# Kernel tuning notes

Measured on AMD Instinct MI355X. Metric: run time of the kernel, lower is better.

The kernel has to match this reference:

```python
import jax, jax.numpy as jnp
import numpy as np

H = 1024   # hiddenDim
L = 3      # numLayers


def _cell(x, h, c, Wih, Whh, bih, bhh):
    """One LSTM cell step, PyTorch gate order (i, f, g, o)."""
    gates = x @ Wih.T + bih + h @ Whh.T + bhh
    i, f, g, o = jnp.split(gates, 4, axis=-1)
    c = jax.nn.sigmoid(f) * c + jax.nn.sigmoid(i) * jnp.tanh(g)
    h = jax.nn.sigmoid(o) * jnp.tanh(c)
    return h, c


def _layer(xs, Wih, Whh, bih, bhh):
    """Run one LSTM layer over a full [B, T, in] sequence; returns (hs [B,T,H], hT, cT).
    Input-to-gate GEMM is hoisted out of the scan for efficiency."""
    B = xs.shape[0]
    Hd = Whh.shape[1]
    xg = jnp.einsum('bti,gi->btg', xs, Wih) + bih  # [B, T, 4H]

    def step(carry, xg_t):
        h, c = carry
        gates = xg_t + h @ Whh.T + bhh
        i, f, g, o = jnp.split(gates, 4, axis=-1)
        c = jax.nn.sigmoid(f) * c + jax.nn.sigmoid(i) * jnp.tanh(g)
        h = jax.nn.sigmoid(o) * jnp.tanh(c)
        return (h, c), h

    h0 = jnp.zeros((B, Hd), xs.dtype)
    (hT, cT), hs = jax.lax.scan(step, (h0, h0), jnp.swapaxes(xg, 0, 1))
    return jnp.swapaxes(hs, 0, 1), hT, cT


def setup_inputs() -> dict:
    key = jax.random.key(0)
    ks = iter(jax.random.split(key, 32))
    B, T, I = 128, 512, 32
    s = 1.0 / np.sqrt(H)

    def u(shape):
        return jax.random.uniform(next(ks), shape, jnp.float32, -s, s)

    return dict(
        x=jax.random.normal(next(ks), (B, T, I), jnp.float32),
        y=jax.random.normal(next(ks), (B, T), jnp.float32),
        force=jax.random.randint(next(ks), (T - 1,), 0, 2, jnp.int32),
        # encoder LSTM (layer 0 takes inputDim, layers 1.. take H)
        enc_Wih0=u((4 * H, I)), enc_Whh0=u((4 * H, H)), enc_bih0=u((4 * H,)), enc_bhh0=u((4 * H,)),
        enc_Wih=u((L - 1, 4 * H, H)), enc_Whh=u((L - 1, 4 * H, H)),
        enc_bih=u((L - 1, 4 * H)), enc_bhh=u((L - 1, 4 * H)),
        # decoder LSTM (layer 0 takes outputDim=1)
        dec_Wih0=u((4 * H, 1)), dec_Whh0=u((4 * H, H)), dec_bih0=u((4 * H,)), dec_bhh0=u((4 * H,)),
        dec_Wih=u((L - 1, 4 * H, H)), dec_Whh=u((L - 1, 4 * H, H)),
        dec_bih=u((L - 1, 4 * H)), dec_bhh=u((L - 1, 4 * H)),
        # unembedding Linear(H, 1)
        Wu=u((1, H)), bu=u((1,)),
    )


def reference(x, y, force,
              enc_Wih0, enc_Whh0, enc_bih0, enc_bhh0,
              enc_Wih, enc_Whh, enc_bih, enc_bhh,
              dec_Wih0, dec_Whh0, dec_bih0, dec_bhh0,
              dec_Wih, dec_Whh, dec_bih, dec_bhh,
              Wu, bu):
    B = x.shape[0]
    # ---- encoder: 3-layer LSTM over x, keep final (h, c) of each layer ----
    hs_f, cs_f = [], []
    xs, hT, cT = _layer(x, enc_Wih0, enc_Whh0, enc_bih0, enc_bhh0)
    hs_f.append(hT); cs_f.append(cT)
    for l in range(L - 1):
        xs, hT, cT = _layer(xs, enc_Wih[l], enc_Whh[l], enc_bih[l], enc_bhh[l])
        hs_f.append(hT); cs_f.append(cT)
    hs = jnp.stack(hs_f)  # [L, B, H]
    cs = jnp.stack(cs_f)

    # ---- decoder: single-step LSTM unrolled via scan, teacher forcing per flag ----
    y3 = y[:, :, None]  # [B, T, 1]
    dec_params = [(dec_Wih0, dec_Whh0, dec_bih0, dec_bhh0)] + \
                 [(dec_Wih[l], dec_Whh[l], dec_bih[l], dec_bhh[l]) for l in range(L - 1)]

    def step(carry, inp):
        x_in, h_all, c_all = carry      # x_in [B,1]
        y_t, f = inp                    # y_t [B,1], f scalar int
        xcur = x_in
        nh, nc = [], []
        for l, (Wih, Whh, bih, bhh) in enumerate(dec_params):
            h, c = _cell(xcur, h_all[l], c_all[l], Wih, Whh, bih, bhh)
            nh.append(h); nc.append(c)
            xcur = h
        out = xcur @ Wu.T + bu          # [B,1] unembedding
        nxt = jnp.where(f > 0, y_t, out)  # teacher forcing branch
        return (nxt, jnp.stack(nh), jnp.stack(nc)), out

    init = (y3[:, 0], hs, cs)
    _, outs = jax.lax.scan(step, init, (jnp.swapaxes(y3[:, 1:], 0, 1), force))
    # output[:, 0] stays zeros as in the torch code
    output = jnp.concatenate([jnp.zeros((B, 1, 1), x.dtype), jnp.swapaxes(outs, 0, 1)], axis=1)
    return output
```

## Files before the change

kernel.cpp:

```cpp
#include <hip/hip_runtime.h>

typedef _Float16 f16;
typedef _Float16 half8 __attribute__((ext_vector_type(8)));
typedef float floatx4 __attribute__((ext_vector_type(4)));

#define HD 1024
#define HSZ (128*1024)

#define LRED(w2,col,row) ((w2)*2304 + (col)*72 + (row))

__device__ __forceinline__ float sigf(float v){ return 1.0f/(1.0f + __expf(-v)); }
__device__ __forceinline__ float tanh_fast(float v){
  float a = fabsf(v);
  float e = __expf(-2.0f*a);
  float t = (1.0f - e)/(1.0f + e);
  return v < 0.0f ? -t : t;
}

__device__ __forceinline__ void st_h16(const f16* p, float hn){
  unsigned v = (unsigned)__builtin_bit_cast(unsigned short, (f16)hn);
  asm volatile("global_store_short %0, %1, off sc0 sc1" :: "v"(p), "v"(v) : "memory");
}
__device__ __forceinline__ void st_f32(const float* p, float v){
  asm volatile("global_store_dword %0, %1, off sc0 sc1" :: "v"(p), "v"(v) : "memory");
}

#define BAR_FLAG_STRIDE 16
#define BAR_EPOCH_OFF   4096

__device__ __forceinline__ void grpbar(unsigned* bar, unsigned target,
                                       int grp, int jb, int tid){
  asm volatile("s_waitcnt vmcnt(0)" ::: "memory");
  __syncthreads();
  if (jb != 0) {
    if (tid == 0) {
      __hip_atomic_store(bar + (grp*128 + jb)*BAR_FLAG_STRIDE, target,
                         __ATOMIC_RELAXED, __HIP_MEMORY_SCOPE_AGENT);
      __builtin_amdgcn_fence(__ATOMIC_ACQUIRE, "agent");
      unsigned* ep = bar + BAR_EPOCH_OFF + (grp*8 + (jb & 7))*BAR_FLAG_STRIDE;
      while (__hip_atomic_load(ep, __ATOMIC_RELAXED, __HIP_MEMORY_SCOPE_AGENT) < target)
        __builtin_amdgcn_s_sleep(1);
    }
  } else {
    if (tid < 64) {
      if (tid == 0) __builtin_amdgcn_fence(__ATOMIC_ACQUIRE, "agent");
      unsigned* f1 = bar + (grp*128 + tid)*BAR_FLAG_STRIDE;
      unsigned* f2 = bar + (grp*128 + 64 + tid)*BAR_FLAG_STRIDE;
      for (;;) {
        unsigned a = (tid == 0) ? target
                   : __hip_atomic_load(f1, __ATOMIC_RELAXED, __HIP_MEMORY_SCOPE_AGENT);
        unsigned b = __hip_atomic_load(f2, __ATOMIC_RELAXED, __HIP_MEMORY_SCOPE_AGENT);
        if (__all(a >= target && b >= target)) break;
        __builtin_amdgcn_s_sleep(1);
      }
      if (tid < 8)
        __hip_atomic_store(bar + BAR_EPOCH_OFF + (grp*8 + tid)*BAR_FLAG_STRIDE, target,
                           __ATOMIC_RELAXED, __HIP_MEMORY_SCOPE_AGENT);
    }
  }
  __syncthreads();
}

__global__ void permB(const float* __restrict__ S1, int K1,
                      const float* __restrict__ S2, int K2,
                      f16* __restrict__ dst, int KT, long total)
{
  long idx = (long)blockIdx.x*blockDim.x + threadIdx.x;
  if (idx >= total) return;
  int lane = idx & 63; long r1 = idx >> 6;
  int kt = (int)(r1 % KT); r1 /= KT;
  int nt = (int)(r1 & 1);  r1 >>= 1;
  int w  = (int)(r1 & 7);  int jb = (int)(r1 >> 3);
  int n = lane & 15, q = lane >> 4;
  int colidx = nt*16 + n;
  int g = colidx >> 3, dj = colidx & 7;
  int row = g*1024 + jb*8 + dj;
  int kbase = w*(KT*32) + kt*32 + q*8;
  f16* d = dst + (size_t)idx*8;
  #pragma unroll
  for (int i = 0; i < 8; ++i) {
    int k = kbase + i;
    float v = (k < K1) ? S1[(size_t)row*K1 + k] : S2[(size_t)row*K2 + (k - K1)];
    d[i] = (f16)v;
  }
}

__global__ void permW0(const float* __restrict__ W, f16* __restrict__ dst){
  int idx = blockIdx.x*blockDim.x + threadIdx.x;
  if (idx >= 1024*128) return;
  int k = idx & 31, g = (idx >> 5) & 3, j = idx >> 7;
  dst[idx] = (f16)W[(size_t)(g*1024 + j)*32 + k];
}

__global__ void addvec(const float* __restrict__ a, const float* __restrict__ b,
                       float* __restrict__ o, int nel){
  int i = blockIdx.x*blockDim.x + threadIdx.x;
  if (i < nel) o[i] = a[i] + b[i];
}

__global__ void cvtf16(const float* __restrict__ a, f16* __restrict__ o, long nel){
  long i = (long)blockIdx.x*blockDim.x + threadIdx.x;
  if (i < nel) o[i] = (f16)a[i];
}

__global__ void zero_hc(f16* __restrict__ hb, unsigned* __restrict__ bar){
  long i = (long)blockIdx.x*blockDim.x + threadIdx.x;
  if (i < 3L*2*HSZ) hb[i] = (f16)0.f;
  if (i < 8192)     bar[i] = 0u;
}

template<int KT>
__device__ __forceinline__ void loadB(half8* Bl, const f16* __restrict__ Bp,
                                      int jb, int w, int lane){
  const f16* src = Bp + ((size_t)(jb*8 + w))*(2*KT)*512 + (size_t)lane*8;
  #pragma unroll
  for (int f = 0; f < 2*KT; ++f)
    Bl[f] = *(const half8*)(src + (size_t)f*512);
}

template<int KT, int XM, int PM>
__device__ __forceinline__ void run_unit(
    const half8* Bl,
    const f16* __restrict__ A1, const f16* __restrict__ A2,
    float& creg, f16* __restrict__ hout, const float* __restrict__ bl,
    const f16* __restrict__ x16r, const f16* __restrict__ W0pp, int t,
    const float* xsp, const float* __restrict__ w0cp,
    const float* __restrict__ Wup, float* __restrict__ partialp, int jb,
    float* lds_red, int r0, int j0, int w, int lane, int tid)
{
  const int n = lane & 15, q = lane >> 4;
  const int k0 = w * (KT*32);
  const f16* Aw = (KT == 8 && w >= 4) ? (A2 + (k0 - 1024)) : (A1 + k0);

  floatx4 acc[4][2] = {};
  #pragma unroll
  for (int kt = 0; kt < KT; ++kt) {
    half8 a[4];
    #pragma unroll
    for (int mt = 0; mt < 4; ++mt)
      a[mt] = *(const half8*)(Aw + (size_t)(r0 + mt*16 + n)*HD + (kt*32 + q*8));
    #pragma unroll
    for (int mt = 0; mt < 4; ++mt) {
      acc[mt][0] = __builtin_amdgcn_mfma_f32_16x16x32_f16(a[mt], Bl[kt],      acc[mt][0], 0, 0, 0);
      acc[mt][1] = __builtin_amdgcn_mfma_f32_16x16x32_f16(a[mt], Bl[KT + kt], acc[mt][1], 0, 0, 0);
    }
  }

  __syncthreads();
  if (w >= 4) {
    #pragma unroll
    for (int mt = 0; mt < 4; ++mt)
      #pragma unroll
      for (int nt = 0; nt < 2; ++nt) {
        int base = LRED(w-4, nt*16 + n, mt*16 + q*4);
        #pragma unroll
        for (int r = 0; r < 4; ++r) lds_red[base + r] = acc[mt][nt][r];
      }
  }
  __syncthreads();
  if (w < 4) {
    #pragma unroll
    for (int mt = 0; mt < 4; ++mt)
      #pragma unroll
      for (int nt = 0; nt < 2; ++nt) {
        int base = LRED(w, nt*16 + n, mt*16 + q*4);
        #pragma unroll
        for (int r = 0; r < 4; ++r)
          lds_red[base + r] += acc[mt][nt][r];
      }
  }
  __syncthreads();

  const int rrow = tid >> 3, rdj = tid & 7;
  const int rg = r0 + rrow;
  const int j  = j0 + rdj;
  float g4[4];
  #pragma unroll
  for (int gi = 0; gi < 4; ++gi) {
    const int col = gi*8 + rdj;
    float s = bl[gi*1024 + j];
    #pragma unroll
    for (int w2 = 0; w2 < 4; ++w2) s += lds_red[LRED(w2, col, rrow)];
    g4[gi] = s;
  }
  if (XM == 1) {
    const f16* xr = x16r + ((size_t)rg*512 + t)*32;
    const f16* wj = W0pp + (size_t)j*128;
    #pragma unroll
    for (int k = 0; k < 32; ++k) {
      float xk = (float)xr[k];
      g4[0] += xk * (float)wj[k];
      g4[1] += xk * (float)wj[32+k];
      g4[2] += xk * (float)wj[64+k];
      g4[3] += xk * (float)wj[96+k];
    }
  }
  if (XM == 2) {
    float xv = xsp[rrow];
    g4[0] += xv * w0cp[j];       g4[1] += xv * w0cp[1024+j];
    g4[2] += xv * w0cp[2048+j];  g4[3] += xv * w0cp[3072+j];
  }
  float iv = sigf(g4[0]), fv = sigf(g4[1]);
  float gv = tanh_fast(g4[2]), ov = sigf(g4[3]);
  float cn = fv*creg + iv*gv;
  creg = cn;
  float hn = ov * tanh_fast(cn);
  st_h16(hout + ((size_t)rg*HD + j), hn);
  if (PM == 1) {
    float pv = hn * Wup[j];
    pv += __shfl_xor(pv, 1); pv += __shfl_xor(pv, 2); pv += __shfl_xor(pv, 4);
    if ((lane & 7) == 0) st_f32(partialp + jb*128 + rg, pv);
  }
}

#define HB(l,pp)  (hbuf + ((size_t)((l)*2 + (pp)))*HSZ)

__global__ void __launch_bounds__(512)
__attribute__((amdgpu_waves_per_eu(2, 2)))
persist(
    const f16* __restrict__ Bp_e0, const f16* __restrict__ Bp_e1, const f16* __restrict__ Bp_e2,
    const f16* __restrict__ Bp_d0, const f16* __restrict__ Bp_d1, const f16* __restrict__ Bp_d2,
    const float* __restrict__ biases, const f16* __restrict__ x16, const f16* __restrict__ W0p,
    const float* __restrict__ w0c, const float* __restrict__ Wu, const float* __restrict__ bu_p,
    const float* __restrict__ y, const int* __restrict__ force,
    f16* __restrict__ hbuf,
    float* __restrict__ partial, float* __restrict__ dout,
    unsigned* __restrict__ bar)
{
  unsigned ep = 0;

  const int cu = blockIdx.x;
  const int xgrp = cu & 7;
  const int mh = (xgrp >> 2) & 1;
  const int jb = (cu >> 3) * 4 + (xgrp & 3);
  const int r0 = mh*64, j0 = jb*8;
  const int tid = threadIdx.x;
  const int w = tid >> 6, lane = tid & 63;

  __shared__ float lds_red[4*2304];
  __shared__ float lds_x[512];
  __shared__ float xs[64];

  half8 B0[8], B1[16], B2[16];
  float c0 = 0.f, c1 = 0.f, c2 = 0.f;

  loadB<4>(B0, Bp_e0, jb, w, lane);
  loadB<8>(B1, Bp_e1, jb, w, lane);
  loadB<8>(B2, Bp_e2, jb, w, lane);

  for (int s = 0; s < 514; ++s) {
    if (s < 512) {
      int t = s, p = t & 1;
      run_unit<4,1,0>(B0, HB(0,1-p), nullptr, c0, HB(0,p), biases,
                      x16, W0p, t, nullptr, nullptr, nullptr, nullptr, 0,
                      lds_red, r0, j0, w, lane, tid);
    }
    {
      int t = s - 1;
      if (t >= 0 && t < 512) {
        int p = t & 1;
        run_unit<8,0,0>(B1, HB(0,p), HB(1,1-p), c1, HB(1,p), biases + 4096,
                        nullptr, nullptr, 0, nullptr, nullptr, nullptr, nullptr, 0,
                        lds_red, r0, j0, w, lane, tid);
      }
    }
    {
      int t = s - 2;
      if (t >= 0 && t < 512) {
        int p = t & 1;
        run_unit<8,0,0>(B2, HB(1,p), HB(2,1-p), c2, HB(2,p), biases + 2*4096,
                        nullptr, nullptr, 0, nullptr, nullptr, nullptr, nullptr, 0,
                        lds_red, r0, j0, w, lane, tid);
      }
    }
    grpbar(bar, ++ep, mh, jb, tid);
  }

  loadB<4>(B0, Bp_d0, jb, w, lane);
  loadB<8>(B1, Bp_d1, jb, w, lane);
  loadB<8>(B2, Bp_d2, jb, w, lane);

  for (int t = 0; t < 511; ++t) {
    const int p = t & 1;
    if (t > 0) {
      int seg = tid >> 6, rowx = tid & 63;
      float s = 0.f;
      const float* pp = partial + r0 + rowx;
      for (int jj = seg*16; jj < seg*16 + 16; ++jj) s += pp[jj*128];
      lds_x[seg*64 + rowx] = s;
    }
    __syncthreads();
    if (tid < 64) {
      float xv;
      if (t == 0) {
        if (jb == 0) st_f32(dout + (size_t)(r0+tid)*512, 0.0f);
        xv = y[(size_t)(r0+tid)*512];
      } else {
        float ov = bu_p[0];
        #pragma unroll
        for (int sg = 0; sg < 8; ++sg) ov += lds_x[sg*64 + tid];
        if (jb == 0) st_f32(dout + (size_t)(r0+tid)*512 + t, ov);
        xv = (force[t-1] > 0) ? y[(size_t)(r0+tid)*512 + t] : ov;
      }
      xs[tid] = xv;
    }
    run_unit<4,2,0>(B0, HB(0,1-p), nullptr, c0, HB(0,p), biases + 3*4096,
                    nullptr, nullptr, 0, xs, w0c, nullptr, nullptr, 0,
                    lds_red, r0, j0, w, lane, tid);
    grpbar(bar, ++ep, mh, jb, tid);
    run_unit<8,0,0>(B1, HB(0,p), HB(1,1-p), c1, HB(1,p), biases + 4*4096,
                    nullptr, nullptr, 0, nullptr, nullptr, nullptr, nullptr, 0,
                    lds_red, r0, j0, w, lane, tid);
    grpbar(bar, ++ep, mh, jb, tid);
    run_unit<8,0,1>(B2, HB(1,p), HB(2,1-p), c2, HB(2,p), biases + 5*4096,
                    nullptr, nullptr, 0, nullptr, nullptr, Wu, partial, jb,
                    lds_red, r0, j0, w, lane, tid);
    grpbar(bar, ++ep, mh, jb, tid);
  }

  if (jb == 0 && tid < 64) {
    float ov = bu_p[0];
    for (int jj = 0; jj < 128; ++jj) ov += partial[jj*128 + r0 + tid];
    st_f32(dout + (size_t)(r0+tid)*512 + 511, ov);
  }
}

extern "C" void kernel_launch(void* const* d_in, const int* in_sizes, int n_in,
                              void* d_out, int out_size, void* d_ws, size_t ws_size,
                              hipStream_t stream)
{
  const float* x     = (const float*)d_in[0];
  const float* y     = (const float*)d_in[1];
  const int*   force = (const int*)  d_in[2];
  const float* eWih0 = (const float*)d_in[3];
  const float* eWhh0 = (const float*)d_in[4];
  const float* ebih0 = (const float*)d_in[5];
  const float* ebhh0 = (const float*)d_in[6];
  const float* eWih  = (const float*)d_in[7];
  const float* eWhh  = (const float*)d_in[8];
  const float* ebih  = (const float*)d_in[9];
  const float* ebhh  = (const float*)d_in[10];
  const float* dWih0 = (const float*)d_in[11];
  const float* dWhh0 = (const float*)d_in[12];
  const float* dbih0 = (const float*)d_in[13];
  const float* dbhh0 = (const float*)d_in[14];
  const float* dWih  = (const float*)d_in[15];
  const float* dWhh  = (const float*)d_in[16];
  const float* dbih  = (const float*)d_in[17];
  const float* dbhh  = (const float*)d_in[18];
  const float* Wu    = (const float*)d_in[19];
  const float* bu    = (const float*)d_in[20];
  float* out = (float*)d_out;

  char* ws = (char*)d_ws;
  size_t off = 0;
  auto alloc = [&](size_t bytes)->void* {
    void* pp = ws + off; off += (bytes + 255) & ~(size_t)255; return pp;
  };
  f16* Bp_e0 = (f16*)alloc(4096ULL*1024*2);
  f16* Bp_e1 = (f16*)alloc(4096ULL*2048*2);
  f16* Bp_e2 = (f16*)alloc(4096ULL*2048*2);
  f16* Bp_d0 = (f16*)alloc(4096ULL*1024*2);
  f16* Bp_d1 = (f16*)alloc(4096ULL*2048*2);
  f16* Bp_d2 = (f16*)alloc(4096ULL*2048*2);
  float* biases = (float*)alloc(6ULL*4096*4);
  f16* x16  = (f16*)alloc(128ULL*512*32*2);
  f16* W0p  = (f16*)alloc(1024ULL*128*2);
  f16* hbuf = (f16*)alloc(3ULL*2*HSZ*2);
  float* partialb = (float*)alloc(128ULL*128*4);
  unsigned* bar = (unsigned*)alloc(32*1024);
  (void)ws_size; (void)in_sizes; (void)n_in; (void)out_size;

  const int THR = 256;
  auto blocks = [&](long nel){ return dim3((unsigned)((nel + THR - 1)/THR)); };

  long tot4 = 128L*8*2*4*64, tot8 = 128L*8*2*8*64;
  hipLaunchKernelGGL(permB, blocks(tot4), dim3(THR), 0, stream,
                     eWhh0, 1024, eWhh0, 1024, Bp_e0, 4, tot4);
  hipLaunchKernelGGL(permB, blocks(tot8), dim3(THR), 0, stream,
                     eWih, 1024, eWhh, 1024, Bp_e1, 8, tot8);
  hipLaunchKernelGGL(permB, blocks(tot8), dim3(THR), 0, stream,
                     eWih + 4096L*1024, 1024, eWhh + 4096L*1024, 1024, Bp_e2, 8, tot8);
  hipLaunchKernelGGL(permB, blocks(tot4), dim3(THR), 0, stream,
                     dWhh0, 1024, dWhh0, 1024, Bp_d0, 4, tot4);
  hipLaunchKernelGGL(permB, blocks(tot8), dim3(THR), 0, stream,
                     dWih, 1024, dWhh, 1024, Bp_d1, 8, tot8);
  hipLaunchKernelGGL(permB, blocks(tot8), dim3(THR), 0, stream,
                     dWih + 4096L*1024, 1024, dWhh + 4096L*1024, 1024, Bp_d2, 8, tot8);
  hipLaunchKernelGGL(permW0, blocks(1024L*128), dim3(THR), 0, stream, eWih0, W0p);

  hipLaunchKernelGGL(addvec, blocks(4096), dim3(THR), 0, stream, ebih0, ebhh0, biases + 0*4096, 4096);
  hipLaunchKernelGGL(addvec, blocks(4096), dim3(THR), 0, stream, ebih, ebhh, biases + 1*4096, 4096);
  hipLaunchKernelGGL(addvec, blocks(4096), dim3(THR), 0, stream, ebih + 4096, ebhh + 4096, biases + 2*4096, 4096);
  hipLaunchKernelGGL(addvec, blocks(4096), dim3(THR), 0, stream, dbih0, dbhh0, biases + 3*4096, 4096);
  hipLaunchKernelGGL(addvec, blocks(4096), dim3(THR), 0, stream, dbih, dbhh, biases + 4*4096, 4096);
  hipLaunchKernelGGL(addvec, blocks(4096), dim3(THR), 0, stream, dbih + 4096, dbhh + 4096, biases + 5*4096, 4096);

  hipLaunchKernelGGL(cvtf16, blocks(128L*512*32), dim3(THR), 0, stream, x, x16, 128L*512*32);
  hipLaunchKernelGGL(zero_hc, blocks(3L*2*HSZ), dim3(THR), 0, stream, hbuf, bar);

  void* kargs[] = {
    (void*)&Bp_e0, (void*)&Bp_e1, (void*)&Bp_e2,
    (void*)&Bp_d0, (void*)&Bp_d1, (void*)&Bp_d2,
    (void*)&biases, (void*)&x16, (void*)&W0p,
    (void*)&dWih0, (void*)&Wu, (void*)&bu,
    (void*)&y, (void*)&force,
    (void*)&hbuf, (void*)&partialb, (void*)&out,
    (void*)&bar
  };
  hipLaunchCooperativeKernel((const void*)persist, dim3(256), dim3(512), kargs, 0, stream);
}
```

Before: 39.96 ms.

## Quad-buffer hidden states and issue acquire fence only every third barrier

Grows the hidden-state ring from 2 to 4 slots per layer so a slot is not reused until several barriers later. This lets the acquire fence (cache invalidate) in the group barrier run only on every third epoch instead of every barrier, on the assumption that stale cache lines cannot hold data from a slot still in use. It also caps the spin loops with an iteration bound. The risk is correctness: skipping invalidation may let blocks read stale h values from non-coherent caches, and the spin cap could silently break the barrier if a wait runs long.

```diff
diff --git a/kernel.cpp b/kernel.cpp
--- a/kernel.cpp
+++ b/kernel.cpp
@@ -27,26 +27,32 @@
 
 #define BAR_FLAG_STRIDE 16
 #define BAR_EPOCH_OFF   4096
+#define SPIN_CAP (1u<<20)
 
 __device__ __forceinline__ void grpbar(unsigned* bar, unsigned target,
-                                       int grp, int jb, int tid){
+                                       int grp, int jb, int tid, bool doinv){
   asm volatile("s_waitcnt vmcnt(0)" ::: "memory");
   __syncthreads();
   if (jb != 0) {
     if (tid == 0) {
       __hip_atomic_store(bar + (grp*128 + jb)*BAR_FLAG_STRIDE, target,
                          __ATOMIC_RELAXED, __HIP_MEMORY_SCOPE_AGENT);
-      __builtin_amdgcn_fence(__ATOMIC_ACQUIRE, "agent");
-      unsigned* ep = bar + BAR_EPOCH_OFF + (grp*8 + (jb & 7))*BAR_FLAG_STRIDE;
-      while (__hip_atomic_load(ep, __ATOMIC_RELAXED, __HIP_MEMORY_SCOPE_AGENT) < target)
+      if (doinv)
+        __builtin_amdgcn_fence(__ATOMIC_ACQUIRE, "agent");
+      unsigned* epp = bar + BAR_EPOCH_OFF + (grp*8 + (jb & 7))*BAR_FLAG_STRIDE;
+      for (unsigned it = 0; it < SPIN_CAP; ++it) {
+        if (__hip_atomic_load(epp, __ATOMIC_RELAXED, __HIP_MEMORY_SCOPE_AGENT) >= target)
+          break;
         __builtin_amdgcn_s_sleep(1);
+      }
     }
   } else {
     if (tid < 64) {
-      if (tid == 0) __builtin_amdgcn_fence(__ATOMIC_ACQUIRE, "agent");
+      if (tid == 0 && doinv)
+        __builtin_amdgcn_fence(__ATOMIC_ACQUIRE, "agent");
       unsigned* f1 = bar + (grp*128 + tid)*BAR_FLAG_STRIDE;
       unsigned* f2 = bar + (grp*128 + 64 + tid)*BAR_FLAG_STRIDE;
-      for (;;) {
+      for (unsigned it = 0; it < SPIN_CAP; ++it) {
         unsigned a = (tid == 0) ? target
                    : __hip_atomic_load(f1, __ATOMIC_RELAXED, __HIP_MEMORY_SCOPE_AGENT);
         unsigned b = __hip_atomic_load(f2, __ATOMIC_RELAXED, __HIP_MEMORY_SCOPE_AGENT);
@@ -105,7 +111,7 @@
 
 __global__ void zero_hc(f16* __restrict__ hb, unsigned* __restrict__ bar){
   long i = (long)blockIdx.x*blockDim.x + threadIdx.x;
-  if (i < 3L*2*HSZ) hb[i] = (f16)0.f;
+  if (i < 3L*4*HSZ) hb[i] = (f16)0.f;
   if (i < 8192)     bar[i] = 0u;
 }
 
@@ -213,7 +219,7 @@
   }
 }
 
-#define HB(l,pp)  (hbuf + ((size_t)((l)*2 + (pp)))*HSZ)
+#define HB(l,slot)  (hbuf + ((size_t)((l)*4 + (slot)))*HSZ)
 
 __global__ void __launch_bounds__(512)
 __attribute__((amdgpu_waves_per_eu(2, 2)))
@@ -250,16 +256,15 @@
 
   for (int s = 0; s < 514; ++s) {
     if (s < 512) {
-      int t = s, p = t & 1;
-      run_unit<4,1,0>(B0, HB(0,1-p), nullptr, c0, HB(0,p), biases,
+      int t = s;
+      run_unit<4,1,0>(B0, HB(0,(t+3)&3), nullptr, c0, HB(0,t&3), biases,
                       x16, W0p, t, nullptr, nullptr, nullptr, nullptr, 0,
                       lds_red, r0, j0, w, lane, tid);
     }
     {
       int t = s - 1;
       if (t >= 0 && t < 512) {
-        int p = t & 1;
-        run_unit<8,0,0>(B1, HB(0,p), HB(1,1-p), c1, HB(1,p), biases + 4096,
+        run_unit<8,0,0>(B1, HB(0,t&3), HB(1,(t+3)&3), c1, HB(1,t&3), biases + 4096,
                         nullptr, nullptr, 0, nullptr, nullptr, nullptr, nullptr, 0,
                         lds_red, r0, j0, w, lane, tid);
       }
@@ -267,13 +272,13 @@
     {
       int t = s - 2;
       if (t >= 0 && t < 512) {
-        int p = t & 1;
-        run_unit<8,0,0>(B2, HB(1,p), HB(2,1-p), c2, HB(2,p), biases + 2*4096,
+        run_unit<8,0,0>(B2, HB(1,t&3), HB(2,(t+3)&3), c2, HB(2,t&3), biases + 2*4096,
                         nullptr, nullptr, 0, nullptr, nullptr, nullptr, nullptr, 0,
                         lds_red, r0, j0, w, lane, tid);
       }
     }
-    grpbar(bar, ++ep, mh, jb, tid);
+    ++ep;
+    grpbar(bar, ep, mh, jb, tid, (ep % 3u) == 1u);
   }
 
   loadB<4>(B0, Bp_d0, jb, w, lane);
@@ -281,7 +286,6 @@
   loadB<8>(B2, Bp_d2, jb, w, lane);
 
   for (int t = 0; t < 511; ++t) {
-    const int p = t & 1;
     if (t > 0) {
       int seg = tid >> 6, rowx = tid & 63;
       float s = 0.f;
@@ -304,18 +308,18 @@
       }
       xs[tid] = xv;
     }
-    run_unit<4,2,0>(B0, HB(0,1-p), nullptr, c0, HB(0,p), biases + 3*4096,
+    run_unit<4,2,0>(B0, HB(0,(t+3)&3), nullptr, c0, HB(0,t&3), biases + 3*4096,
                     nullptr, nullptr, 0, xs, w0c, nullptr, nullptr, 0,
                     lds_red, r0, j0, w, lane, tid);
-    grpbar(bar, ++ep, mh, jb, tid);
-    run_unit<8,0,0>(B1, HB(0,p), HB(1,1-p), c1, HB(1,p), biases + 4*4096,
+    ++ep; grpbar(bar, ep, mh, jb, tid, (ep % 3u) == 1u);
+    run_unit<8,0,0>(B1, HB(0,t&3), HB(1,(t+3)&3), c1, HB(1,t&3), biases + 4*4096,
                     nullptr, nullptr, 0, nullptr, nullptr, nullptr, nullptr, 0,
                     lds_red, r0, j0, w, lane, tid);
-    grpbar(bar, ++ep, mh, jb, tid);
-    run_unit<8,0,1>(B2, HB(1,p), HB(2,1-p), c2, HB(2,p), biases + 5*4096,
+    ++ep; grpbar(bar, ep, mh, jb, tid, (ep % 3u) == 1u);
+    run_unit<8,0,1>(B2, HB(1,t&3), HB(2,(t+3)&3), c2, HB(2,t&3), biases + 5*4096,
                     nullptr, nullptr, 0, nullptr, nullptr, Wu, partial, jb,
                     lds_red, r0, j0, w, lane, tid);
-    grpbar(bar, ++ep, mh, jb, tid);
+    ++ep; grpbar(bar, ep, mh, jb, tid, (ep % 3u) == 1u);
   }
 
   if (jb == 0 && tid < 64) {
@@ -366,7 +370,7 @@
   float* biases = (float*)alloc(6ULL*4096*4);
   f16* x16  = (f16*)alloc(128ULL*512*32*2);
   f16* W0p  = (f16*)alloc(1024ULL*128*2);
-  f16* hbuf = (f16*)alloc(3ULL*2*HSZ*2);
+  f16* hbuf = (f16*)alloc(3ULL*4*HSZ*2);
   float* partialb = (float*)alloc(128ULL*128*4);
   unsigned* bar = (unsigned*)alloc(32*1024);
   (void)ws_size; (void)in_sizes; (void)n_in; (void)out_size;
@@ -397,7 +401,7 @@
   hipLaunchKernelGGL(addvec, blocks(4096), dim3(THR), 0, stream, dbih + 4096, dbhh + 4096, biases + 5*4096, 4096);
 
   hipLaunchKernelGGL(cvtf16, blocks(128L*512*32), dim3(THR), 0, stream, x, x16, 128L*512*32);
-  hipLaunchKernelGGL(zero_hc, blocks(3L*2*HSZ), dim3(THR), 0, stream, hbuf, bar);
+  hipLaunchKernelGGL(zero_hc, blocks(3L*4*HSZ), dim3(THR), 0, stream, hbuf, bar);
 
   void* kargs[] = {
     (void*)&Bp_e0, (void*)&Bp_e1, (void*)&Bp_e2,
```

Result: faster. 38.35 ms (-4.0%).
